# Kernel optimization log

Hardware: AMD Instinct MI355X
Metric: run time of the kernel (lower is better)

The kernel has to match this reference:

```python
import jax, jax.numpy as jnp
import numpy as np

# Compressed weight shape [O, I] represents a dense [m=2*O, k=2*I] matrix:
#  - 1:2 structured row sparsity: `indices` [O] gives the nonzero dense row ids
#  - 2:4 structured col sparsity: `metadata` [O, I] gives, for each compressed
#    element, its position (0..3) within its group of 4 dense columns
O, I = 4096, 2048          # compressed weight dims (out_features, in_features)
M_DIM, K_DIM = 2 * O, 2 * I  # dense GEMM dims m, k
N_TOK = 4096               # n = input.shape[0]
K_ACT = 2048               # number of active activation rows (multiple of 64)
PAD_MULT = 64


def setup_inputs() -> dict:
    key = jax.random.key(0)
    k1, k2, k3, k4, k5 = jax.random.split(key, 5)
    inp = jax.random.normal(k1, (N_TOK, K_ACT), dtype=jnp.float32)
    # unique, sorted active-feature indices into the dense k dimension
    idx = jnp.sort(jax.random.permutation(k2, K_DIM)[:K_ACT]).astype(jnp.int32)
    # compressed N:M weight values (original uses torch.rand -> uniform [0,1))
    weight = jax.random.uniform(k3, (O, I), dtype=jnp.float32)
    # 1:2 row sparsity: which O of the m dense rows are nonzero
    indices = jnp.sort(jax.random.permutation(k4, M_DIM)[:O]).astype(jnp.int32)
    # 2:4 metadata: per group of 4 dense columns, 2 distinct sorted positions
    G = I // 2
    scores = jax.random.uniform(k5, (O, G, 4))
    metadata = jnp.sort(jnp.argsort(scores, axis=-1)[..., :2], axis=-1)
    metadata = metadata.reshape(O, I).astype(jnp.int32)
    return {"input": inp, "idx": idx, "weight": weight,
            "indices": indices, "metadata": metadata}


def _padding_idx(idx, mult):
    # pad index list to a multiple of `mult` (static shapes)
    pad = (-idx.shape[0]) % mult
    return jnp.pad(idx, (0, pad)), pad


def reference(input, idx, weight, indices, metadata):
    O_, I_ = weight.shape
    m, k, n = 2 * O_, 2 * I_, input.shape[0]
    # ---- decompress N:M weight to dense [m, k] ----
    group_base = (jnp.arange(I_) // 2) * 4                 # [I]
    dense_cols = group_base[None, :] + metadata            # [O, I] in [0, k)
    W = jnp.zeros((m, k), weight.dtype).at[indices[:, None], dense_cols].set(weight)
    # ---- decompress sparse activation to dense B [k, n] ----
    idx_p, pad = _padding_idx(idx, PAD_MULT)
    vals = jnp.pad(input, ((0, 0), (0, pad)))              # [n, K_act+pad]
    B = jnp.zeros((k, n), input.dtype).at[idx_p].add(vals.T)
    # ---- sparse-sparse GEMM (dense-equivalent reference) ----
    return W @ B                                           # [m, n]
```

## Files before the change

### kernel.cpp

```cpp
#include <hip/hip_runtime.h>
#include <hip/hip_bf16.h>
#include <stdint.h>

#define O_DIM   4096
#define I_DIM   2048
#define M_DENSE 8192
#define K_DENSE 4096
#define N_TOK   4096
#define K_ACT   2048

typedef __bf16 bf16x8 __attribute__((ext_vector_type(8)));
typedef float  f32x4  __attribute__((ext_vector_type(4)));

__device__ __forceinline__ unsigned f2bf(float f) {
    unsigned u = __builtin_bit_cast(unsigned, f);
    return (u + 0x7FFFu + ((u >> 16) & 1u)) >> 16;
}

__device__ __forceinline__ void load16(const unsigned short* g, unsigned short* l) {
    __builtin_amdgcn_global_load_lds(
        (__attribute__((address_space(1))) void*)(g),
        (__attribute__((address_space(3))) void*)(l),
        16, 0, 0);
}

__global__ void zero_inactive(const int* __restrict__ indices, float4* __restrict__ out4) {
    int b = blockIdx.x;
    int lo = (b == 0) ? -1 : indices[b - 1];
    int hi = (b == O_DIM) ? M_DENSE : indices[b];
    for (int row = lo + 1; row < hi; ++row) {
        float4* dst = out4 + (size_t)row * (N_TOK / 4);
        for (int c = threadIdx.x; c < N_TOK / 4; c += 256)
            dst[c] = float4{0.f, 0.f, 0.f, 0.f};
    }
}

__global__ __launch_bounds__(256) void decompress_w(const float* __restrict__ weight,
                                                    const int* __restrict__ metadata,
                                                    const int* __restrict__ idx,
                                                    uint4* __restrict__ A2) {
    __shared__ int   smeta[I_DIM];
    __shared__ float sw[I_DIM];
    int o = blockIdx.x;
    const int4*   mrow = (const int4*)(metadata + (size_t)o * I_DIM);
    const float4* wrow = (const float4*)(weight + (size_t)o * I_DIM);
#pragma unroll
    for (int it = 0; it < I_DIM / 4 / 256; ++it) {
        int i = it * 256 + threadIdx.x;
        *(int4*)(smeta + i * 4) = mrow[i];
        *(float4*)(sw + i * 4)  = wrow[i];
    }
    __syncthreads();
    int j0 = threadIdx.x * 8;
    int4 c0 = *(const int4*)(idx + j0);
    int4 c1 = *(const int4*)(idx + j0 + 4);
    int cs[8] = {c0.x, c0.y, c0.z, c0.w, c1.x, c1.y, c1.z, c1.w};
    unsigned r[8];
#pragma unroll
    for (int u = 0; u < 8; ++u) {
        int c = cs[u];
        int g2 = (c >> 2) * 2;
        int pos = c & 3;
        int m0v = smeta[g2], m1v = smeta[g2 + 1];
        float v = (m0v == pos) ? sw[g2] : ((m1v == pos) ? sw[g2 + 1] : 0.0f);
        r[u] = f2bf(v);
    }
    uint4 packed;
    packed.x = r[0] | (r[1] << 16);
    packed.y = r[2] | (r[3] << 16);
    packed.z = r[4] | (r[5] << 16);
    packed.w = r[6] | (r[7] << 16);
    A2[((size_t)o * K_ACT + j0) >> 3] = packed;
}

__global__ void cast_b(const float4* __restrict__ in, uint4* __restrict__ outb) {
    int gid = blockIdx.x * blockDim.x + threadIdx.x;
    float4 a = in[2 * gid], b = in[2 * gid + 1];
    uint4 u;
    u.x = f2bf(a.x) | (f2bf(a.y) << 16);
    u.y = f2bf(a.z) | (f2bf(a.w) << 16);
    u.z = f2bf(b.x) | (f2bf(b.y) << 16);
    u.w = f2bf(b.z) | (f2bf(b.w) << 16);
    outb[gid] = u;
}

__global__ void gemm_scatter(const unsigned short* __restrict__ A,
                             const unsigned short* __restrict__ Bt,
                             const int* __restrict__ indices,
                             float* __restrict__ out) {
    constexpr int N = N_TOK, K = K_ACT;
    constexpr int TM = 128, TN = 128, BK = 32;
    __shared__ alignas(16) unsigned short sA[TM * BK];
    __shared__ alignas(16) unsigned short sB[TN * BK];

    const int t    = threadIdx.x;
    const int wave = t >> 6;
    const int lane = t & 63;
    const int m0 = blockIdx.y * TM;
    const int n0 = blockIdx.x * TN;

    const int fa0 = t, fa1 = t + 256;
    const unsigned short* gA0 = A  + (size_t)(m0 + (fa0 >> 2)) * K + (fa0 & 3) * 8;
    const unsigned short* gA1 = A  + (size_t)(m0 + (fa1 >> 2)) * K + (fa1 & 3) * 8;
    const unsigned short* gB0 = Bt + (size_t)(n0 + (fa0 >> 2)) * K + (fa0 & 3) * 8;
    const unsigned short* gB1 = Bt + (size_t)(n0 + (fa1 >> 2)) * K + (fa1 & 3) * 8;

    unsigned short* lA0 = sA + wave * 512;
    unsigned short* lA1 = sA + 2048 + wave * 512;
    unsigned short* lB0 = sB + wave * 512;
    unsigned short* lB1 = sB + 2048 + wave * 512;

    const int wm   = (wave >> 1) * 64;
    const int wn   = (wave & 1) * 64;
    const int quad = lane >> 4;
    const int lr   = lane & 15;
    const int kq   = quad * 8;

    f32x4 acc[4][4] = {};

    for (int kk = 0; kk < K; kk += BK) {
        __syncthreads();
        load16(gA0 + kk, lA0);
        load16(gA1 + kk, lA1);
        load16(gB0 + kk, lB0);
        load16(gB1 + kk, lB1);
        __syncthreads();

        bf16x8 af[4], bf[4];
#pragma unroll
        for (int mi = 0; mi < 4; ++mi)
            af[mi] = *(const bf16x8*)(sA + (wm + mi * 16 + lr) * BK + kq);
#pragma unroll
        for (int ni = 0; ni < 4; ++ni)
            bf[ni] = *(const bf16x8*)(sB + (wn + ni * 16 + lr) * BK + kq);
#pragma unroll
        for (int mi = 0; mi < 4; ++mi)
#pragma unroll
            for (int ni = 0; ni < 4; ++ni)
                acc[mi][ni] = __builtin_amdgcn_mfma_f32_16x16x32_bf16(
                    af[mi], bf[ni], acc[mi][ni], 0, 0, 0);
    }

#pragma unroll
    for (int mi = 0; mi < 4; ++mi) {
#pragma unroll
        for (int r = 0; r < 4; ++r) {
            int gm = m0 + wm + mi * 16 + quad * 4 + r;
            int orow = indices[gm];
            float* op = out + (size_t)orow * N + n0 + wn + lr;
#pragma unroll
            for (int ni = 0; ni < 4; ++ni)
                op[ni * 16] = acc[mi][ni][r];
        }
    }
}

extern "C" void kernel_launch(void* const* d_in, const int* in_sizes, int n_in,
                              void* d_out, int out_size, void* d_ws, size_t ws_size,
                              hipStream_t stream) {
    const float* input    = (const float*)d_in[0];
    const int*   idx      = (const int*)d_in[1];
    const float* weight   = (const float*)d_in[2];
    const int*   indices  = (const int*)d_in[3];
    const int*   metadata = (const int*)d_in[4];
    float* out = (float*)d_out;

    unsigned short* A2  = (unsigned short*)d_ws;
    unsigned short* Bbt = (unsigned short*)((char*)d_ws + (size_t)(16 << 20));

    zero_inactive<<<O_DIM + 1, 256, 0, stream>>>(indices, (float4*)out);
    decompress_w<<<O_DIM, 256, 0, stream>>>(weight, metadata, idx, (uint4*)A2);
    cast_b<<<(N_TOK * K_ACT / 8) / 256, 256, 0, stream>>>((const float4*)input, (uint4*)Bbt);

    dim3 grid(N_TOK / 128, O_DIM / 128);
    gemm_scatter<<<grid, 256, 0, stream>>>(A2, Bbt, indices, out);
}
```

Baseline: 296.3 us.

## Fuse prep kernels and move inactive-row zeroing into GEMM blocks

Merges weight decompression and the activation bf16 cast into one launch, with block index selecting the role. Drops the separate zero_inactive kernel: each GEMM block binary-searches the indices to find the inactive dense rows in its 256-row span and zeroes its 128-column slice of them. This cuts two kernel launches and lets the zero writes overlap GEMM work. It also adds launch_bounds(256,4) to the GEMM, which may constrain registers. The cost is an extra prologue with a binary search, shared atomics and two block barriers in every GEMM block.

```diff
diff --git a/kernel.cpp b/kernel.cpp
--- a/kernel.cpp
+++ b/kernel.cpp
@@ -24,21 +24,24 @@
         16, 0, 0);
 }
 
-__global__ void zero_inactive(const int* __restrict__ indices, float4* __restrict__ out4) {
-    int b = blockIdx.x;
-    int lo = (b == 0) ? -1 : indices[b - 1];
-    int hi = (b == O_DIM) ? M_DENSE : indices[b];
-    for (int row = lo + 1; row < hi; ++row) {
-        float4* dst = out4 + (size_t)row * (N_TOK / 4);
-        for (int c = threadIdx.x; c < N_TOK / 4; c += 256)
-            dst[c] = float4{0.f, 0.f, 0.f, 0.f};
+__global__ __launch_bounds__(256) void prep(const float* __restrict__ weight,
+                                            const int* __restrict__ metadata,
+                                            const int* __restrict__ idx,
+                                            const float* __restrict__ input,
+                                            uint4* __restrict__ A2,
+                                            uint4* __restrict__ Bbt) {
+    if (blockIdx.x >= O_DIM) {
+        int gid = (blockIdx.x - O_DIM) * 256 + threadIdx.x;
+        const float4* in = (const float4*)input;
+        float4 a = in[2 * gid], b = in[2 * gid + 1];
+        uint4 u;
+        u.x = f2bf(a.x) | (f2bf(a.y) << 16);
+        u.y = f2bf(a.z) | (f2bf(a.w) << 16);
+        u.z = f2bf(b.x) | (f2bf(b.y) << 16);
+        u.w = f2bf(b.z) | (f2bf(b.w) << 16);
+        Bbt[gid] = u;
+        return;
     }
-}
-
-__global__ __launch_bounds__(256) void decompress_w(const float* __restrict__ weight,
-                                                    const int* __restrict__ metadata,
-                                                    const int* __restrict__ idx,
-                                                    uint4* __restrict__ A2) {
     __shared__ int   smeta[I_DIM];
     __shared__ float sw[I_DIM];
     int o = blockIdx.x;
@@ -73,31 +76,41 @@
     A2[((size_t)o * K_ACT + j0) >> 3] = packed;
 }
 
-__global__ void cast_b(const float4* __restrict__ in, uint4* __restrict__ outb) {
-    int gid = blockIdx.x * blockDim.x + threadIdx.x;
-    float4 a = in[2 * gid], b = in[2 * gid + 1];
-    uint4 u;
-    u.x = f2bf(a.x) | (f2bf(a.y) << 16);
-    u.y = f2bf(a.z) | (f2bf(a.w) << 16);
-    u.z = f2bf(b.x) | (f2bf(b.y) << 16);
-    u.w = f2bf(b.z) | (f2bf(b.w) << 16);
-    outb[gid] = u;
-}
-
-__global__ void gemm_scatter(const unsigned short* __restrict__ A,
-                             const unsigned short* __restrict__ Bt,
-                             const int* __restrict__ indices,
-                             float* __restrict__ out) {
+__global__ __launch_bounds__(256, 4) void gemm_scatter(
+        const unsigned short* __restrict__ A,
+        const unsigned short* __restrict__ Bt,
+        const int* __restrict__ indices,
+        float* __restrict__ out) {
     constexpr int N = N_TOK, K = K_ACT;
     constexpr int TM = 128, TN = 128, BK = 32;
     __shared__ alignas(16) unsigned short sA[TM * BK];
     __shared__ alignas(16) unsigned short sB[TN * BK];
+    __shared__ int s_list[256];
+    __shared__ int s_cnt;
 
     const int t    = threadIdx.x;
     const int wave = t >> 6;
     const int lane = t & 63;
     const int m0 = blockIdx.y * TM;
     const int n0 = blockIdx.x * TN;
+
+    {
+        if (t == 0) s_cnt = 0;
+        int r = blockIdx.y * 256 + t;
+        int lo = 0, hi = O_DIM;
+        while (lo < hi) { int mid = (lo + hi) >> 1; if (indices[mid] < r) lo = mid + 1; else hi = mid; }
+        bool inactive = !(lo < O_DIM && indices[lo] == r);
+        __syncthreads();
+        if (inactive) { int p = atomicAdd(&s_cnt, 1); s_list[p] = r; }
+        __syncthreads();
+        int nin = s_cnt;
+        float4 z4 = {0.f, 0.f, 0.f, 0.f};
+        for (int task = t; task < nin * 32; task += 256) {
+            int row = s_list[task >> 5];
+            int c4  = task & 31;
+            *(float4*)(out + (size_t)row * N + n0 + c4 * 4) = z4;
+        }
+    }
 
     const int fa0 = t, fa1 = t + 256;
     const unsigned short* gA0 = A  + (size_t)(m0 + (fa0 >> 2)) * K + (fa0 & 3) * 8;
@@ -168,9 +181,8 @@
     unsigned short* A2  = (unsigned short*)d_ws;
     unsigned short* Bbt = (unsigned short*)((char*)d_ws + (size_t)(16 << 20));
 
-    zero_inactive<<<O_DIM + 1, 256, 0, stream>>>(indices, (float4*)out);
-    decompress_w<<<O_DIM, 256, 0, stream>>>(weight, metadata, idx, (uint4*)A2);
-    cast_b<<<(N_TOK * K_ACT / 8) / 256, 256, 0, stream>>>((const float4*)input, (uint4*)Bbt);
+    prep<<<O_DIM + (N_TOK * K_ACT / 8) / 256, 256, 0, stream>>>(
+        weight, metadata, idx, input, (uint4*)A2, (uint4*)Bbt);
 
     dim3 grid(N_TOK / 128, O_DIM / 128);
     gemm_scatter<<<grid, 256, 0, stream>>>(A2, Bbt, indices, out);
```

Measured after the change: 291.2 us. No clear change (-1.7%).
